# Optimization experiments

Measured on AMD Instinct MI355X. Metric: run time of the kernel, lower is better.

## Reference

```python
import jax, jax.numpy as jnp
import numpy as np

EPS = 1e-5


def _sqdist(x):
    # x: (B, D, N) -> pairwise squared distances (B, N, N)
    sq = jnp.sum(x * x, axis=1)                    # (B, N)
    g = jnp.einsum('bdn,bdm->bnm', x, x)           # (B, N, N)
    return jnp.maximum(sq[:, :, None] + sq[:, None, :] - 2.0 * g, 0.0)


def _spatialnorm(emb):
    # normalize over node dim per (batch, feature)
    m = emb.mean(axis=2, keepdims=True)
    v = emb.var(axis=2, keepdims=True)
    return (emb - m) / jnp.sqrt(v + EPS)


def _gopconv(adj, deg, emb, w, bias, wres, bres):
    # emb: (B, F, N); adj: (B, N, N); deg: (B, N)
    adj_msg = jnp.einsum('bfn,bnm->bfm', emb, adj)         # adjacency operator
    deg_msg = emb * deg[:, None, :]                        # diagonal degree operator
    cat = jnp.concatenate([deg_msg, adj_msg], axis=1)      # (B, 2F, N)
    conv = jnp.einsum('of,bfn->bon', w, cat) + bias[None, :, None]
    res = jnp.einsum('of,bfn->bon', wres, emb) + bres[None, :, None]
    return jax.nn.relu(conv) + res


def setup_inputs() -> dict:
    key = jax.random.key(0)
    ks = jax.random.split(key, 12)
    B, N, F0, F, L, DK = 4, 2048, 6, 64, 2, 16
    s = 0.1  # weight scale to keep learned-adjacency distances moderate
    return {
        'emb_in': jax.random.normal(ks[0], (B, F0, N), jnp.float32),
        'sigma': jnp.ones((1,), jnp.float32),
        'fst_w': jax.random.normal(ks[1], (F, 2 * F0), jnp.float32) * s,
        'fst_b': jax.random.normal(ks[2], (F,), jnp.float32) * s,
        'fst_wres': jax.random.normal(ks[3], (F, F0), jnp.float32) * s,
        'fst_bres': jax.random.normal(ks[4], (F,), jnp.float32) * s,
        'adj_proj': jax.random.normal(ks[5], (L, DK, F), jnp.float32) * s,
        'w': jax.random.normal(ks[6], (L, F, 2 * F), jnp.float32) * s,
        'b': jax.random.normal(ks[7], (L, F), jnp.float32) * s,
        'wres': jax.random.normal(ks[8], (L, F, F), jnp.float32) * s,
        'bres': jax.random.normal(ks[9], (L, F), jnp.float32) * s,
        'fcl_w': jax.random.normal(ks[10], (1, F), jnp.float32) * s,
        'fcl_b': jax.random.normal(ks[11], (1,), jnp.float32) * s,
    }


def reference(emb_in, sigma, fst_w, fst_b, fst_wres, fst_bres,
              adj_proj, w, b, wres, bres, fcl_w, fcl_b):
    # Gaussian kernel on input features -> dense adjacency (B, N, N)
    adj = jnp.exp(-_sqdist(emb_in) / (sigma[0] ** 2))
    deg = adj.sum(axis=2)
    emb = _gopconv(adj, deg, emb_in, fst_w, fst_b, fst_wres, fst_bres)
    L = w.shape[0]
    for i in range(L):  # fixed small layer count
        proj = jnp.einsum('df,bfn->bdn', adj_proj[i], emb)  # learned adjacency kernel
        adj = jnp.exp(-_sqdist(proj))
        deg = adj.sum(axis=2)
        emb = _gopconv(adj, deg, _spatialnorm(emb), w[i], b[i], wres[i], bres[i])
    pooled = emb.mean(axis=2)  # readout over nodes -> (B, F)
    # InstanceNorm1d(1) on (B, 1, F): normalize over feature dim per sample
    m = pooled.mean(axis=1, keepdims=True)
    v = pooled.var(axis=1, keepdims=True)
    normed = (pooled - m) / jnp.sqrt(v + EPS)
    logits = normed @ fcl_w.T + fcl_b  # (B, 1)
    return jax.nn.sigmoid(logits[:, 0])
```

## Files before the change

kernel.cpp:

```cpp
#include <hip/hip_runtime.h>
#include <hip/hip_bf16.h>
#include <math.h>

namespace {

constexpr int B  = 4;
constexpr int N  = 2048;
constexpr int F0 = 6;
constexpr int F  = 64;
constexpr int DK = 16;
constexpr float EPS = 1e-5f;
constexpr int MT   = N / 64;
constexpr int NCH  = 4;

typedef float fx4 __attribute__((ext_vector_type(4)));
typedef __attribute__((ext_vector_type(8)))  short bf16x8;
typedef __attribute__((ext_vector_type(4)))  short bf16x4;
typedef __attribute__((ext_vector_type(16))) float f32x16;

__device__ inline short f2bf(float x, float* xr) {
  __hip_bfloat16 h = __float2bfloat16(x);
  *xr = __bfloat162float(h);
  short s; __builtin_memcpy(&s, &h, 2);
  return s;
}
__device__ inline short f2bf(float x) {
  __hip_bfloat16 h = __float2bfloat16(x);
  short s; __builtin_memcpy(&s, &h, 2);
  return s;
}
__device__ inline float bf2f(short s) {
  unsigned int u = ((unsigned int)(unsigned short)s) << 16;
  float f; __builtin_memcpy(&f, &u, 4);
  return f;
}

template<int FIN, bool NORM, bool XBF>
__global__ __launch_bounds__(256) void k_wx(const float* __restrict__ Xf,
                                            const short* __restrict__ Xb,
                                            const float* __restrict__ sigma,
                                            const float* __restrict__ ssum,
                                            const float* __restrict__ ssq,
                                            const float* __restrict__ Wc,
                                            const float* __restrict__ Wr,
                                            const float* __restrict__ Ap,
                                            short* __restrict__ Tq,
                                            short* __restrict__ Tbf,
                                            short* __restrict__ projT,
                                            float* __restrict__ sqnb) {
  int z = blockIdx.z, b = blockIdx.y, n0 = blockIdx.x * 64;
  int t = threadIdx.x, n = t & 63, og = t >> 6;
  __shared__ float xS[64][FIN + 1];
  __shared__ __align__(16) float wT[FIN][68];
  __shared__ float mnS[64], rsS[64];
  __shared__ float sp[4][64];
  for (int e = t; e < FIN * 64; e += 256) {
    int f = e >> 6, nn = e & 63;
    float v = XBF ? bf2f(Xb[((size_t)b * FIN + f) * N + n0 + nn])
                  : Xf[((size_t)b * FIN + f) * N + n0 + nn];
    xS[nn][f] = v;
  }
  bool l0proj = (z == 3 && Ap == nullptr);
  if (!l0proj) {
    const float* base; int ld, off, OUT;
    if (z == 0)      { base = Wc; ld = 2 * FIN; off = 0;   OUT = 64; }
    else if (z == 1) { base = Wc; ld = 2 * FIN; off = FIN; OUT = 64; }
    else if (z == 2) { base = Wr; ld = FIN;     off = 0;   OUT = 64; }
    else             { base = Ap; ld = FIN;     off = 0;   OUT = DK; }
    for (int e = t; e < OUT * FIN; e += 256) {
      int o = e / FIN, f = e - o * FIN;
      wT[f][o] = base[(size_t)o * ld + off + f];
    }
  }
  if (NORM && z < 3 && t < 64) {
    int row = b * FIN + t;
    float S = ssum[2 * row] + ssum[2 * row + 1];
    float Q = ssq[2 * row] + ssq[2 * row + 1];
    float mn = S / (float)N;
    mnS[t] = mn;
    rsS[t] = rsqrtf(Q / (float)N - mn * mn + EPS);
  }
  __syncthreads();
  if (z < 3) {
    float cacc[16] = {};
#pragma unroll 4
    for (int f = 0; f < FIN; ++f) {
      float x = xS[n][f];
      if (NORM) x = (x - mnS[f]) * rsS[f];
      fx4 w0 = *(const fx4*)&wT[f][og * 16 + 0];
      fx4 w1 = *(const fx4*)&wT[f][og * 16 + 4];
      fx4 w2 = *(const fx4*)&wT[f][og * 16 + 8];
      fx4 w3 = *(const fx4*)&wT[f][og * 16 + 12];
#pragma unroll
      for (int k = 0; k < 4; ++k) {
        cacc[k + 0]  = fmaf(w0[k], x, cacc[k + 0]);
        cacc[k + 4]  = fmaf(w1[k], x, cacc[k + 4]);
        cacc[k + 8]  = fmaf(w2[k], x, cacc[k + 8]);
        cacc[k + 12] = fmaf(w3[k], x, cacc[k + 12]);
      }
    }
    if (z == 1) {
#pragma unroll
      for (int k = 0; k < 16; ++k)
        Tbf[((size_t)b * 64 + og * 16 + k) * N + n0 + n] = f2bf(cacc[k]);
    } else {
      int sl = (z == 0) ? 0 : 1;
#pragma unroll
      for (int k = 0; k < 16; ++k)
        Tq[(((size_t)b * 2 + sl) * 64 + og * 16 + k) * N + n0 + n] = f2bf(cacc[k]);
    }
  } else {
    float r[4];
    bf16x4 hv;
    if (Ap != nullptr) {
      float cacc[4] = {};
#pragma unroll 4
      for (int f = 0; f < FIN; ++f) {
        float x = xS[n][f];
        fx4 w0 = *(const fx4*)&wT[f][og * 4];
#pragma unroll
        for (int k = 0; k < 4; ++k) cacc[k] = fmaf(w0[k], x, cacc[k]);
      }
#pragma unroll
      for (int k = 0; k < 4; ++k) hv[k] = f2bf(cacc[k], &r[k]);
    } else {
      float inv = 1.f / sigma[0];
#pragma unroll
      for (int k = 0; k < 4; ++k) {
        int d = og * 4 + k;
        float v = (d < F0) ? xS[n][d] * inv : 0.f;
        hv[k] = f2bf(v, &r[k]);
      }
    }
    *(bf16x4*)&projT[((size_t)b * N + n0 + n) * DK + og * 4] = hv;
    float s = 0.f;
#pragma unroll
    for (int k = 0; k < 4; ++k) s = fmaf(r[k], r[k], s);
    sp[og][n] = s;
    __syncthreads();
    if (t < 64) sqnb[(size_t)b * N + n0 + t] = sp[0][t] + sp[1][t] + sp[2][t] + sp[3][t];
  }
}

__global__ __launch_bounds__(256, 4) void k_adjmsg(const short* __restrict__ projT,
                                                   const float* __restrict__ sqnb,
                                                   const short* __restrict__ Tbf,
                                                   short* __restrict__ pdmsg,
                                                   float* __restrict__ pdeg) {
  constexpr int NCb = N / NCH;
  constexpr int CPX = NCH * B / 8;
  int i = blockIdx.x;
  int xcd = i & 7;
  int j = i >> 3;
  int lc = j / MT;
  int mtile = j - lc * MT;
  int combo = xcd * CPX + lc;
  int ch = combo >> 2;
  int b  = combo & 3;
  int M0 = mtile * 64;
  int n0 = ch * NCb;

  int t = threadIdx.x;
  int w = t >> 6, l = t & 63;
  int l31 = l & 31, lh = l >> 5;
  int mq = w & 1, nq = w >> 1;
  int fq = w & 1, mq2 = w >> 1;

  const short* pbT = projT + (size_t)b * N * DK;
  const short* vb = Tbf + (size_t)b * F * N;
  const float* sq = sqnb + (size_t)b * N;

  __shared__ __align__(16) short adjT[2][64][68];
  __shared__ __align__(16) short vS[2][64][68];
  __shared__ float sqmS[64];
  __shared__ float degS[2][64];

  int am = l31 + 32 * mq;
  bf16x8 afrag = *(const bf16x8*)&pbT[(size_t)(M0 + am) * DK + lh * 8];
  if (t < 64) sqmS[t] = sq[M0 + t];
  __syncthreads();
  float sqmr[16];
#pragma unroll
  for (int r = 0; r < 16; ++r)
    sqmr[r] = sqmS[(r & 3) + 8 * (r >> 2) + 4 * lh + 32 * mq];

  f32x16 acc;
#pragma unroll
  for (int r = 0; r < 16; ++r) acc[r] = 0.f;
  float pdm[16];
#pragma unroll
  for (int r = 0; r < 16; ++r) pdm[r] = 0.f;

  int buf = 0;
  for (int nt = 0; nt < NCb; nt += 64) {
    int bn = l31 + 32 * nq;
    bf16x8 bfrag = *(const bf16x8*)&pbT[(size_t)(n0 + nt + bn) * DK + lh * 8];
    float sqn_v = sq[n0 + nt + bn];
    {
      int f = t >> 2, nb16 = (t & 3) * 16;
#pragma unroll
      for (int jj = 0; jj < 4; ++jj) {
        *(bf16x4*)&vS[buf][f][nb16 + 4 * jj] =
            *(const bf16x4*)&vb[(size_t)f * N + n0 + nt + nb16 + 4 * jj];
      }
    }
    f32x16 gz;
#pragma unroll
    for (int r = 0; r < 16; ++r) gz[r] = 0.f;
    f32x16 g = __builtin_amdgcn_mfma_f32_32x32x16_bf16(afrag, bfrag, gz, 0, 0, 0);
#pragma unroll
    for (int r = 0; r < 16; ++r) {
      int m = (r & 3) + 8 * (r >> 2) + 4 * lh + 32 * mq;
      float dist = fmaxf(sqmr[r] + sqn_v - 2.f * g[r], 0.f);
      float a = __expf(-dist);
      pdm[r] += a;
      adjT[buf][m][bn] = f2bf(a);
    }
    __syncthreads();
#pragma unroll
    for (int kk = 0; kk < 4; ++kk) {
      int nb = kk * 16 + lh * 8;
      int fA = l31 + 32 * fq;
      int mB = l31 + 32 * mq2;
      bf16x4 alo = *(const bf16x4*)&vS[buf][fA][nb];
      bf16x4 ahi = *(const bf16x4*)&vS[buf][fA][nb + 4];
      bf16x4 blo = *(const bf16x4*)&adjT[buf][mB][nb];
      bf16x4 bhi = *(const bf16x4*)&adjT[buf][mB][nb + 4];
      bf16x8 af2, bf2;
#pragma unroll
      for (int i2 = 0; i2 < 4; ++i2) {
        af2[i2] = alo[i2]; af2[i2 + 4] = ahi[i2];
        bf2[i2] = blo[i2]; bf2[i2 + 4] = bhi[i2];
      }
      acc = __builtin_amdgcn_mfma_f32_32x32x16_bf16(af2, bf2, acc, 0, 0, 0);
    }
    buf ^= 1;
  }
#pragma unroll
  for (int r = 0; r < 16; ++r) {
    pdm[r] += __shfl_xor(pdm[r], 1);
    pdm[r] += __shfl_xor(pdm[r], 2);
    pdm[r] += __shfl_xor(pdm[r], 4);
    pdm[r] += __shfl_xor(pdm[r], 8);
    pdm[r] += __shfl_xor(pdm[r], 16);
  }
  if (l31 == 0) {
#pragma unroll
    for (int r = 0; r < 16; ++r)
      degS[nq][(r & 3) + 8 * (r >> 2) + 4 * lh + 32 * mq] = pdm[r];
  }
  __syncthreads();
  if (t < 64) {
    float s = degS[0][t] + degS[1][t];
    __builtin_nontemporal_store(s, &pdeg[(size_t)combo * N + M0 + t]);
  }
  short* pdm_g = pdmsg + (size_t)combo * F * N;
  int m_out = l31 + 32 * mq2;
#pragma unroll
  for (int r = 0; r < 16; ++r) {
    int f_r = (r & 3) + 8 * (r >> 2) + 4 * lh + 32 * fq;
    __builtin_nontemporal_store(f2bf(acc[r]), &pdm_g[(size_t)f_r * N + M0 + m_out]);
  }
}

__global__ __launch_bounds__(256) void k_ep(const short* __restrict__ pdmsg,
                                            const float* __restrict__ pdeg,
                                            const short* __restrict__ Tq,
                                            const float* __restrict__ bias,
                                            const float* __restrict__ bres,
                                            short* __restrict__ out,
                                            float* __restrict__ ssum,
                                            float* __restrict__ ssq) {
  int t = threadIdx.x;
  int idx = blockIdx.x * 256 + t;
  int row = idx >> 9;
  int c4 = idx & 511;
  int o = row & 63, b = row >> 6;
  fx4 dm = {0.f, 0.f, 0.f, 0.f};
  fx4 dg = {0.f, 0.f, 0.f, 0.f};
#pragma unroll
  for (int c = 0; c < NCH; ++c) {
    bf16x4 pv = __builtin_nontemporal_load(
        &((const bf16x4*)pdmsg)[(((size_t)c * B + b) * 64 + o) * 512 + c4]);
#pragma unroll
    for (int j = 0; j < 4; ++j) dm[j] += bf2f(pv[j]);
    dg += ((const fx4*)pdeg)[((size_t)c * B + b) * 512 + c4];
  }
  bf16x4 t0v = ((const bf16x4*)Tq)[(((size_t)b * 2 + 0) * 64 + o) * 512 + c4];
  bf16x4 t2v = ((const bf16x4*)Tq)[(((size_t)b * 2 + 1) * 64 + o) * 512 + c4];
  float bi = bias[o], br = bres[o];
  fx4 ov;
  bf16x4 ob;
#pragma unroll
  for (int j = 0; j < 4; ++j) {
    float v = fmaxf(dm[j] + bf2f(t0v[j]) * dg[j] + bi, 0.f) + bf2f(t2v[j]) + br;
    ov[j] = v;
    ob[j] = f2bf(v);
  }
  ((bf16x4*)out)[((size_t)b * 64 + o) * 512 + c4] = ob;
  float ps = ov[0] + ov[1] + ov[2] + ov[3];
  float pq = fmaf(ov[0], ov[0], fmaf(ov[1], ov[1], fmaf(ov[2], ov[2], ov[3] * ov[3])));
#pragma unroll
  for (int off = 1; off < 64; off <<= 1) {
    ps += __shfl_xor(ps, off);
    pq += __shfl_xor(pq, off);
  }
  __shared__ float r1[4], r2[4];
  if ((t & 63) == 0) { r1[t >> 6] = ps; r2[t >> 6] = pq; }
  __syncthreads();
  if (t == 0) {
    ssum[blockIdx.x] = r1[0] + r1[1] + r1[2] + r1[3];
    ssq[blockIdx.x]  = r2[0] + r2[1] + r2[2] + r2[3];
  }
}

__global__ __launch_bounds__(256) void k_readout(const float* __restrict__ ssum,
                                                 const float* __restrict__ fw,
                                                 const float* __restrict__ fb,
                                                 float* __restrict__ out) {
  int t = threadIdx.x, b = t >> 6, l = t & 63;
  int row = b * 64 + l;
  float po = (ssum[2 * row] + ssum[2 * row + 1]) / (float)N;
  float mn = po;
#pragma unroll
  for (int off = 1; off < 64; off <<= 1) mn += __shfl_xor(mn, off);
  mn *= (1.f / 64.f);
  float d = po - mn;
  float var = d * d;
#pragma unroll
  for (int off = 1; off < 64; off <<= 1) var += __shfl_xor(var, off);
  var *= (1.f / 64.f);
  float rs = rsqrtf(var + EPS);
  float lg = d * rs * fw[l];
#pragma unroll
  for (int off = 1; off < 64; off <<= 1) lg += __shfl_xor(lg, off);
  if (l == 0) out[b] = 1.f / (1.f + __expf(-(lg + fb[0])));
}

}

extern "C" void kernel_launch(void* const* d_in, const int* in_sizes, int n_in,
                              void* d_out, int out_size, void* d_ws, size_t ws_size,
                              hipStream_t stream) {
  const float* emb_in   = (const float*)d_in[0];
  const float* sigma    = (const float*)d_in[1];
  const float* fst_w    = (const float*)d_in[2];
  const float* fst_b    = (const float*)d_in[3];
  const float* fst_wres = (const float*)d_in[4];
  const float* fst_bres = (const float*)d_in[5];
  const float* adj_proj = (const float*)d_in[6];
  const float* w        = (const float*)d_in[7];
  const float* bw       = (const float*)d_in[8];
  const float* wres     = (const float*)d_in[9];
  const float* bres     = (const float*)d_in[10];
  const float* fcl_w    = (const float*)d_in[11];
  const float* fcl_b    = (const float*)d_in[12];

  float* ws = (float*)d_ws;
  float* pdeg  = ws;  ws += (size_t)NCH * B * N;
  short* pdmsg = (short*)ws;  ws += (size_t)NCH * B * F * N / 2;
  short* embA  = (short*)ws;  ws += (size_t)B * F * N / 2;
  short* embB  = (short*)ws;  ws += (size_t)B * F * N / 2;
  short* Tq    = (short*)ws;  ws += (size_t)B * F * N;
  short* Tbf   = (short*)ws;  ws += (size_t)B * F * N / 2;
  short* projT = (short*)ws;  ws += (size_t)B * DK * N / 2;
  float* sqnb  = ws;  ws += (size_t)B * N;
  float* ssum  = ws;  ws += 2 * (size_t)B * F;
  float* ssq   = ws;  ws += 2 * (size_t)B * F;

  constexpr int EPB = (B * F * N / 4) / 256;
  constexpr int AJB = MT * NCH * B;

  k_wx<F0, false, false><<<dim3(N / 64, B, 4), 256, 0, stream>>>(
      emb_in, nullptr, sigma, nullptr, nullptr, fst_w, fst_wres, nullptr,
      Tq, Tbf, projT, sqnb);
  k_adjmsg<<<dim3(AJB), 256, 0, stream>>>(projT, sqnb, Tbf, pdmsg, pdeg);
  k_ep<<<dim3(EPB), 256, 0, stream>>>(pdmsg, pdeg, Tq, fst_b, fst_bres, embA, ssum, ssq);

  const short* src = embA;
  short* dst = embB;
  for (int i = 0; i < 2; ++i) {
    k_wx<F, true, true><<<dim3(N / 64, B, 4), 256, 0, stream>>>(
        nullptr, src, nullptr, ssum, ssq, w + (size_t)i * F * 2 * F,
        wres + (size_t)i * F * F, adj_proj + (size_t)i * DK * F,
        Tq, Tbf, projT, sqnb);
    k_adjmsg<<<dim3(AJB), 256, 0, stream>>>(projT, sqnb, Tbf, pdmsg, pdeg);
    k_ep<<<dim3(EPB), 256, 0, stream>>>(pdmsg, pdeg, Tq, bw + (size_t)i * F,
                                        bres + (size_t)i * F, dst, ssum, ssq);
    short* tmp = (short*)src;
    src = dst;
    dst = tmp;
  }

  k_readout<<<dim3(1), 256, 0, stream>>>(ssum, fcl_w, fcl_b, (float*)d_out);
}
```

Baseline: 81.45 us.

## Merge weight projections, prefetch adjacency tiles into registers, one epilogue block per row

k_wx now computes the degree-weight and residual projections in a single z-slice that shares each normalized input load, so the grid shrinks from four z-slices to three. k_adjmsg loads the next tile's B fragment, squared norms and value vectors into registers before the barrier, overlapping global loads with the MFMA work. k_ep gives each block one whole output row across two halves, which removes the two-part partial sums for ssum/ssq and simplifies the readout. The risks are higher register pressure in k_wx and k_adjmsg, and fewer blocks in k_ep.

```diff
diff --git a/kernel.cpp b/kernel.cpp
--- a/kernel.cpp
+++ b/kernel.cpp
@@ -51,7 +51,7 @@
   int z = blockIdx.z, b = blockIdx.y, n0 = blockIdx.x * 64;
   int t = threadIdx.x, n = t & 63, og = t >> 6;
   __shared__ float xS[64][FIN + 1];
-  __shared__ __align__(16) float wT[FIN][68];
+  __shared__ __align__(16) float wT[FIN][136];
   __shared__ float mnS[64], rsS[64];
   __shared__ float sp[4][64];
   for (int e = t; e < FIN * 64; e += 256) {
@@ -60,28 +60,65 @@
                   : Xf[((size_t)b * FIN + f) * N + n0 + nn];
     xS[nn][f] = v;
   }
-  bool l0proj = (z == 3 && Ap == nullptr);
-  if (!l0proj) {
-    const float* base; int ld, off, OUT;
-    if (z == 0)      { base = Wc; ld = 2 * FIN; off = 0;   OUT = 64; }
-    else if (z == 1) { base = Wc; ld = 2 * FIN; off = FIN; OUT = 64; }
-    else if (z == 2) { base = Wr; ld = FIN;     off = 0;   OUT = 64; }
-    else             { base = Ap; ld = FIN;     off = 0;   OUT = DK; }
-    for (int e = t; e < OUT * FIN; e += 256) {
+  bool l0proj = (z == 2 && Ap == nullptr);
+  if (z == 0) {
+    for (int e = t; e < 64 * FIN; e += 256) {
       int o = e / FIN, f = e - o * FIN;
-      wT[f][o] = base[(size_t)o * ld + off + f];
-    }
-  }
-  if (NORM && z < 3 && t < 64) {
+      wT[f][o] = Wc[(size_t)o * 2 * FIN + f];
+      wT[f][64 + o] = Wr[(size_t)o * FIN + f];
+    }
+  } else if (z == 1) {
+    for (int e = t; e < 64 * FIN; e += 256) {
+      int o = e / FIN, f = e - o * FIN;
+      wT[f][o] = Wc[(size_t)o * 2 * FIN + FIN + f];
+    }
+  } else if (!l0proj) {
+    for (int e = t; e < DK * FIN; e += 256) {
+      int o = e / FIN, f = e - o * FIN;
+      wT[f][o] = Ap[(size_t)o * FIN + f];
+    }
+  }
+  if (NORM && z < 2 && t < 64) {
     int row = b * FIN + t;
-    float S = ssum[2 * row] + ssum[2 * row + 1];
-    float Q = ssq[2 * row] + ssq[2 * row + 1];
+    float S = ssum[row];
+    float Q = ssq[row];
     float mn = S / (float)N;
     mnS[t] = mn;
     rsS[t] = rsqrtf(Q / (float)N - mn * mn + EPS);
   }
   __syncthreads();
-  if (z < 3) {
+  if (z == 0) {
+    float c1[16] = {}, c2[16] = {};
+#pragma unroll 4
+    for (int f = 0; f < FIN; ++f) {
+      float x = xS[n][f];
+      if (NORM) x = (x - mnS[f]) * rsS[f];
+      fx4 w0 = *(const fx4*)&wT[f][og * 16 + 0];
+      fx4 w1 = *(const fx4*)&wT[f][og * 16 + 4];
+      fx4 w2 = *(const fx4*)&wT[f][og * 16 + 8];
+      fx4 w3 = *(const fx4*)&wT[f][og * 16 + 12];
+      fx4 u0 = *(const fx4*)&wT[f][64 + og * 16 + 0];
+      fx4 u1 = *(const fx4*)&wT[f][64 + og * 16 + 4];
+      fx4 u2 = *(const fx4*)&wT[f][64 + og * 16 + 8];
+      fx4 u3 = *(const fx4*)&wT[f][64 + og * 16 + 12];
+#pragma unroll
+      for (int k = 0; k < 4; ++k) {
+        c1[k + 0]  = fmaf(w0[k], x, c1[k + 0]);
+        c1[k + 4]  = fmaf(w1[k], x, c1[k + 4]);
+        c1[k + 8]  = fmaf(w2[k], x, c1[k + 8]);
+        c1[k + 12] = fmaf(w3[k], x, c1[k + 12]);
+        c2[k + 0]  = fmaf(u0[k], x, c2[k + 0]);
+        c2[k + 4]  = fmaf(u1[k], x, c2[k + 4]);
+        c2[k + 8]  = fmaf(u2[k], x, c2[k + 8]);
+        c2[k + 12] = fmaf(u3[k], x, c2[k + 12]);
+      }
+    }
+#pragma unroll
+    for (int k = 0; k < 16; ++k) {
+      Tq[(((size_t)b * 2 + 0) * 64 + og * 16 + k) * N + n0 + n] = f2bf(c1[k]);
+      Tq[(((size_t)b * 2 + 1) * 64 + og * 16 + k) * N + n0 + n] = f2bf(c2[k]);
+    }
+  } else if (z == 1) {
     float cacc[16] = {};
 #pragma unroll 4
     for (int f = 0; f < FIN; ++f) {
@@ -99,16 +136,9 @@
         cacc[k + 12] = fmaf(w3[k], x, cacc[k + 12]);
       }
     }
-    if (z == 1) {
-#pragma unroll
-      for (int k = 0; k < 16; ++k)
-        Tbf[((size_t)b * 64 + og * 16 + k) * N + n0 + n] = f2bf(cacc[k]);
-    } else {
-      int sl = (z == 0) ? 0 : 1;
-#pragma unroll
-      for (int k = 0; k < 16; ++k)
-        Tq[(((size_t)b * 2 + sl) * 64 + og * 16 + k) * N + n0 + n] = f2bf(cacc[k]);
-    }
+#pragma unroll
+    for (int k = 0; k < 16; ++k)
+      Tbf[((size_t)b * 64 + og * 16 + k) * N + n0 + n] = f2bf(cacc[k]);
   } else {
     float r[4];
     bf16x4 hv;
@@ -191,19 +221,20 @@
 #pragma unroll
   for (int r = 0; r < 16; ++r) pdm[r] = 0.f;
 
+  int bn = l31 + 32 * nq;
+  int fV = t >> 2, nb16 = (t & 3) * 16;
+  bf16x8 bfrag = *(const bf16x8*)&pbT[(size_t)(n0 + bn) * DK + lh * 8];
+  float sqn_v = sq[n0 + bn];
+  bf16x4 vreg[4];
+#pragma unroll
+  for (int jj = 0; jj < 4; ++jj)
+    vreg[jj] = *(const bf16x4*)&vb[(size_t)fV * N + n0 + nb16 + 4 * jj];
+
   int buf = 0;
   for (int nt = 0; nt < NCb; nt += 64) {
-    int bn = l31 + 32 * nq;
-    bf16x8 bfrag = *(const bf16x8*)&pbT[(size_t)(n0 + nt + bn) * DK + lh * 8];
-    float sqn_v = sq[n0 + nt + bn];
-    {
-      int f = t >> 2, nb16 = (t & 3) * 16;
-#pragma unroll
-      for (int jj = 0; jj < 4; ++jj) {
-        *(bf16x4*)&vS[buf][f][nb16 + 4 * jj] =
-            *(const bf16x4*)&vb[(size_t)f * N + n0 + nt + nb16 + 4 * jj];
-      }
-    }
+#pragma unroll
+    for (int jj = 0; jj < 4; ++jj)
+      *(bf16x4*)&vS[buf][fV][nb16 + 4 * jj] = vreg[jj];
     f32x16 gz;
 #pragma unroll
     for (int r = 0; r < 16; ++r) gz[r] = 0.f;
@@ -215,6 +246,13 @@
       float a = __expf(-dist);
       pdm[r] += a;
       adjT[buf][m][bn] = f2bf(a);
+    }
+    if (nt + 64 < NCb) {
+      bfrag = *(const bf16x8*)&pbT[(size_t)(n0 + nt + 64 + bn) * DK + lh * 8];
+      sqn_v = sq[n0 + nt + 64 + bn];
+#pragma unroll
+      for (int jj = 0; jj < 4; ++jj)
+        vreg[jj] = *(const bf16x4*)&vb[(size_t)fV * N + n0 + nt + 64 + nb16 + 4 * jj];
     }
     __syncthreads();
 #pragma unroll
@@ -271,35 +309,36 @@
                                             short* __restrict__ out,
                                             float* __restrict__ ssum,
                                             float* __restrict__ ssq) {
+  int row = blockIdx.x;
+  int o = row & 63, b = row >> 6;
   int t = threadIdx.x;
-  int idx = blockIdx.x * 256 + t;
-  int row = idx >> 9;
-  int c4 = idx & 511;
-  int o = row & 63, b = row >> 6;
-  fx4 dm = {0.f, 0.f, 0.f, 0.f};
-  fx4 dg = {0.f, 0.f, 0.f, 0.f};
-#pragma unroll
-  for (int c = 0; c < NCH; ++c) {
-    bf16x4 pv = __builtin_nontemporal_load(
-        &((const bf16x4*)pdmsg)[(((size_t)c * B + b) * 64 + o) * 512 + c4]);
-#pragma unroll
-    for (int j = 0; j < 4; ++j) dm[j] += bf2f(pv[j]);
-    dg += ((const fx4*)pdeg)[((size_t)c * B + b) * 512 + c4];
-  }
-  bf16x4 t0v = ((const bf16x4*)Tq)[(((size_t)b * 2 + 0) * 64 + o) * 512 + c4];
-  bf16x4 t2v = ((const bf16x4*)Tq)[(((size_t)b * 2 + 1) * 64 + o) * 512 + c4];
+  float ps = 0.f, pq = 0.f;
   float bi = bias[o], br = bres[o];
-  fx4 ov;
-  bf16x4 ob;
-#pragma unroll
-  for (int j = 0; j < 4; ++j) {
-    float v = fmaxf(dm[j] + bf2f(t0v[j]) * dg[j] + bi, 0.f) + bf2f(t2v[j]) + br;
-    ov[j] = v;
-    ob[j] = f2bf(v);
-  }
-  ((bf16x4*)out)[((size_t)b * 64 + o) * 512 + c4] = ob;
-  float ps = ov[0] + ov[1] + ov[2] + ov[3];
-  float pq = fmaf(ov[0], ov[0], fmaf(ov[1], ov[1], fmaf(ov[2], ov[2], ov[3] * ov[3])));
+#pragma unroll
+  for (int h = 0; h < 2; ++h) {
+    int c4 = t + h * 256;
+    fx4 dm = {0.f, 0.f, 0.f, 0.f};
+    fx4 dg = {0.f, 0.f, 0.f, 0.f};
+#pragma unroll
+    for (int c = 0; c < NCH; ++c) {
+      bf16x4 pv = __builtin_nontemporal_load(
+          &((const bf16x4*)pdmsg)[(((size_t)c * B + b) * 64 + o) * 512 + c4]);
+#pragma unroll
+      for (int j = 0; j < 4; ++j) dm[j] += bf2f(pv[j]);
+      dg += ((const fx4*)pdeg)[((size_t)c * B + b) * 512 + c4];
+    }
+    bf16x4 t0v = ((const bf16x4*)Tq)[(((size_t)b * 2 + 0) * 64 + o) * 512 + c4];
+    bf16x4 t2v = ((const bf16x4*)Tq)[(((size_t)b * 2 + 1) * 64 + o) * 512 + c4];
+    bf16x4 ob;
+#pragma unroll
+    for (int j = 0; j < 4; ++j) {
+      float v = fmaxf(dm[j] + bf2f(t0v[j]) * dg[j] + bi, 0.f) + bf2f(t2v[j]) + br;
+      ps += v;
+      pq = fmaf(v, v, pq);
+      ob[j] = f2bf(v);
+    }
+    ((bf16x4*)out)[((size_t)b * 64 + o) * 512 + c4] = ob;
+  }
 #pragma unroll
   for (int off = 1; off < 64; off <<= 1) {
     ps += __shfl_xor(ps, off);
@@ -309,8 +348,8 @@
   if ((t & 63) == 0) { r1[t >> 6] = ps; r2[t >> 6] = pq; }
   __syncthreads();
   if (t == 0) {
-    ssum[blockIdx.x] = r1[0] + r1[1] + r1[2] + r1[3];
-    ssq[blockIdx.x]  = r2[0] + r2[1] + r2[2] + r2[3];
+    ssum[row] = r1[0] + r1[1] + r1[2] + r1[3];
+    ssq[row]  = r2[0] + r2[1] + r2[2] + r2[3];
   }
 }
 
@@ -319,8 +358,7 @@
                                                  const float* __restrict__ fb,
                                                  float* __restrict__ out) {
   int t = threadIdx.x, b = t >> 6, l = t & 63;
-  int row = b * 64 + l;
-  float po = (ssum[2 * row] + ssum[2 * row + 1]) / (float)N;
+  float po = ssum[b * 64 + l] / (float)N;
   float mn = po;
 #pragma unroll
   for (int off = 1; off < 64; off <<= 1) mn += __shfl_xor(mn, off);
@@ -365,13 +403,13 @@
   short* Tbf   = (short*)ws;  ws += (size_t)B * F * N / 2;
   short* projT = (short*)ws;  ws += (size_t)B * DK * N / 2;
   float* sqnb  = ws;  ws += (size_t)B * N;
-  float* ssum  = ws;  ws += 2 * (size_t)B * F;
-  float* ssq   = ws;  ws += 2 * (size_t)B * F;
-
-  constexpr int EPB = (B * F * N / 4) / 256;
+  float* ssum  = ws;  ws += (size_t)B * F;
+  float* ssq   = ws;  ws += (size_t)B * F;
+
+  constexpr int EPB = B * F;
   constexpr int AJB = MT * NCH * B;
 
-  k_wx<F0, false, false><<<dim3(N / 64, B, 4), 256, 0, stream>>>(
+  k_wx<F0, false, false><<<dim3(N / 64, B, 3), 256, 0, stream>>>(
       emb_in, nullptr, sigma, nullptr, nullptr, fst_w, fst_wres, nullptr,
       Tq, Tbf, projT, sqnb);
   k_adjmsg<<<dim3(AJB), 256, 0, stream>>>(projT, sqnb, Tbf, pdmsg, pdeg);
@@ -380,7 +418,7 @@
   const short* src = embA;
   short* dst = embB;
   for (int i = 0; i < 2; ++i) {
-    k_wx<F, true, true><<<dim3(N / 64, B, 4), 256, 0, stream>>>(
+    k_wx<F, true, true><<<dim3(N / 64, B, 3), 256, 0, stream>>>(
         nullptr, src, nullptr, ssum, ssq, w + (size_t)i * F * 2 * F,
         wres + (size_t)i * F * F, adj_proj + (size_t)i * DK * F,
         Tq, Tbf, projT, sqnb);
```

After: 81.26 us, median of 2. No clear change (-0.2%).
